# Kernel optimization log

Measured on AMD Instinct MI355X. Metric: run time of the kernel, lower is better.

The kernel has to match this reference:

```python
import jax, jax.numpy as jnp
import numpy as np

KERNEL_SIZE = 7
STRIDE = 1
PADDING = 3
DILATION = 1


def setup_inputs() -> dict:
    key = jax.random.key(0)
    x = jax.random.normal(key, (8, 64, 56, 56), dtype=jnp.float32)
    return {"x": x}


def reference(x):
    """Pairwise subtraction (SAN): center pixel minus each of its k*k
    dilated neighbors, zero-padded borders (pad_mode=0).
    Output: [n, c, k*k, out_h*out_w]."""
    k, s, p, d = KERNEL_SIZE, STRIDE, PADDING, DILATION
    n, c, H, W = x.shape
    out_h = (H + 2 * p - (d * (k - 1) + 1)) // s + 1
    out_w = (W + 2 * p - (d * (k - 1) + 1)) // s + 1
    # centers: unfold with kernel 1, no padding, stride s
    centers = x[:, :, ::s, ::s][:, :, :out_h, :out_w]  # n,c,out_h,out_w
    # neighbors: zero-pad then take k*k strided slices (row-major kernel order
    # to match nn.Unfold)
    xp = jnp.pad(x, ((0, 0), (0, 0), (p, p), (p, p)))
    patches = jnp.stack(
        [
            xp[:, :, i * d : i * d + s * (out_h - 1) + 1 : s,
                     j * d : j * d + s * (out_w - 1) + 1 : s]
            for i in range(k)
            for j in range(k)
        ],
        axis=2,
    )  # n, c, k*k, out_h, out_w
    out = centers.reshape(n, c, 1, out_h * out_w) - patches.reshape(
        n, c, k * k, out_h * out_w
    )
    return out
```

## Files before the change

kernel.cpp:

```cpp
#include <hip/hip_runtime.h>


constexpr int H_ = 56, W_ = 56;
constexpr int KK_  = 49;
constexpr int OHW_ = 3136;
constexpr int PP_  = 63;
constexpr int PR_  = 62;
constexpr int NC_  = 512;
constexpr int LDSN_ = PR_ * PP_;

typedef float f32x4 __attribute__((ext_vector_type(4)));

__global__ __launch_bounds__(256)
void san_kernel(const float* __restrict__ x, float* __restrict__ out) {
    __shared__ float lds[LDSN_];
    const int nc = blockIdx.x;
    const int t  = threadIdx.x;

    #pragma unroll
    for (int i = 0; i < 16; ++i) {
        int j = t + 256 * i;
        if (j < LDSN_) lds[j] = 0.0f;
    }
    __syncthreads();

    const float* plane = x + (size_t)nc * OHW_;

    f32x4 cen0{}, cen1{}, cen2{}, cen3{};
    int ab0 = 0, ab1 = 0, ab2 = 0, ab3 = 0;
    const bool has3 = (t < 16);

#define STAGE(S, CEN, AB)                                           \
    {                                                               \
        int e4 = t + 256 * (S);                                     \
        int oh = e4 / 14, o4 = e4 - oh * 14;                        \
        CEN = *reinterpret_cast<const f32x4*>(plane + e4 * 4);      \
        int lb = (oh + 3) * PP_ + o4 * 4 + 3;                       \
        lds[lb + 0] = CEN[0]; lds[lb + 1] = CEN[1];                 \
        lds[lb + 2] = CEN[2]; lds[lb + 3] = CEN[3];                 \
        AB = oh * PP_ + o4 * 4;                                     \
    }
    STAGE(0, cen0, ab0)
    STAGE(1, cen1, ab1)
    STAGE(2, cen2, ab2)
    if (has3) STAGE(3, cen3, ab3)
#undef STAGE
    __syncthreads();

    float* ob  = out + (size_t)nc * (KK_ * OHW_);
    float* op0 = ob + (size_t)(t      ) * 4;
    float* op1 = ob + (size_t)(t + 256) * 4;
    float* op2 = ob + (size_t)(t + 512) * 4;

    #pragma unroll
    for (int ki = 0; ki < 7; ++ki) {
        #pragma unroll
        for (int kj = 0; kj < 7; ++kj) {
            const int off = ki * PP_ + kj;
            f32x4 r0, r1, r2;
            #pragma unroll
            for (int tt = 0; tt < 4; ++tt) {
                r0[tt] = cen0[tt] - lds[ab0 + off + tt];
                r1[tt] = cen1[tt] - lds[ab1 + off + tt];
                r2[tt] = cen2[tt] - lds[ab2 + off + tt];
            }
            *reinterpret_cast<f32x4*>(op0) = r0;  op0 += OHW_;
            *reinterpret_cast<f32x4*>(op1) = r1;  op1 += OHW_;
            *reinterpret_cast<f32x4*>(op2) = r2;  op2 += OHW_;
        }
    }

    if (has3) {
        float* op3 = ob + (size_t)(t + 768) * 4;
        for (int ki = 0; ki < 7; ++ki) {
            for (int kj = 0; kj < 7; ++kj) {
                int off = ki * PP_ + kj;
                f32x4 r;
                #pragma unroll
                for (int tt = 0; tt < 4; ++tt)
                    r[tt] = cen3[tt] - lds[ab3 + off + tt];
                *reinterpret_cast<f32x4*>(op3) = r;  op3 += OHW_;
            }
        }
    }
}

extern "C" void kernel_launch(void* const* d_in, const int* in_sizes, int n_in,
                              void* d_out, int out_size, void* d_ws, size_t ws_size,
                              hipStream_t stream) {
    const float* x = (const float*)d_in[0];
    float* out = (float*)d_out;
    san_kernel<<<NC_, 256, 0, stream>>>(x, out);
}
```

Measured before the change: 57.44 us.

## Load 12-wide LDS window per row as float4s and reuse across kj

Pads the LDS tile to a 16-byte-aligned pitch with a 4-float halo so staging and neighbor reads become 128-bit LDS accesses. For each kernel row, each thread loads three float4 vectors covering all seven horizontal shifts of its four outputs and reuses them in registers across kj, in place of 196 scalar LDS reads per output group. The separate tail loop for the 16 extra threads is folded into the main unrolled loop with predicated loads and stores. This cuts LDS instruction count, at the cost of more registers and a slightly larger shared buffer.

```diff
diff --git a/kernel.cpp b/kernel.cpp
--- a/kernel.cpp
+++ b/kernel.cpp
@@ -4,46 +4,50 @@
 constexpr int H_ = 56, W_ = 56;
 constexpr int KK_  = 49;
 constexpr int OHW_ = 3136;
-constexpr int PP_  = 63;
-constexpr int PR_  = 62;
 constexpr int NC_  = 512;
-constexpr int LDSN_ = PR_ * PP_;
+constexpr int PITCH = 68;
+constexpr int PROWS = 62;
+constexpr int LHALO = 4;
+constexpr int LDSF  = PROWS * PITCH;
+constexpr int LDS4  = LDSF / 4;
 
 typedef float f32x4 __attribute__((ext_vector_type(4)));
 
+#define WSEL(A, B, C, J) ((J) < 4 ? (A)[(J) & 3] : ((J) < 8 ? (B)[(J) & 3] : (C)[(J) & 3]))
+
 __global__ __launch_bounds__(256)
 void san_kernel(const float* __restrict__ x, float* __restrict__ out) {
-    __shared__ float lds[LDSN_];
+    __shared__ f32x4 lds4[LDS4];
+    float* lds = reinterpret_cast<float*>(lds4);
     const int nc = blockIdx.x;
     const int t  = threadIdx.x;
 
     #pragma unroll
-    for (int i = 0; i < 16; ++i) {
+    for (int i = 0; i < 5; ++i) {
         int j = t + 256 * i;
-        if (j < LDSN_) lds[j] = 0.0f;
+        if (j < LDS4) lds4[j] = f32x4{0.f, 0.f, 0.f, 0.f};
     }
     __syncthreads();
 
     const float* plane = x + (size_t)nc * OHW_;
 
     f32x4 cen0{}, cen1{}, cen2{}, cen3{};
-    int ab0 = 0, ab1 = 0, ab2 = 0, ab3 = 0;
+    int rb0 = 0, rb1 = 0, rb2 = 0, rb3 = 0;
     const bool has3 = (t < 16);
 
-#define STAGE(S, CEN, AB)                                           \
-    {                                                               \
-        int e4 = t + 256 * (S);                                     \
-        int oh = e4 / 14, o4 = e4 - oh * 14;                        \
-        CEN = *reinterpret_cast<const f32x4*>(plane + e4 * 4);      \
-        int lb = (oh + 3) * PP_ + o4 * 4 + 3;                       \
-        lds[lb + 0] = CEN[0]; lds[lb + 1] = CEN[1];                 \
-        lds[lb + 2] = CEN[2]; lds[lb + 3] = CEN[3];                 \
-        AB = oh * PP_ + o4 * 4;                                     \
+#define STAGE(S, CEN, RB)                                            \
+    {                                                                \
+        int e4 = t + 256 * (S);                                      \
+        int oh = e4 / 14, o4 = e4 - oh * 14;                         \
+        CEN = *reinterpret_cast<const f32x4*>(plane + e4 * 4);       \
+        int lb = (oh + 3) * PITCH + LHALO + o4 * 4;                  \
+        *reinterpret_cast<f32x4*>(lds + lb) = CEN;                   \
+        RB = oh * PITCH + (LHALO - 4) + o4 * 4;                      \
     }
-    STAGE(0, cen0, ab0)
-    STAGE(1, cen1, ab1)
-    STAGE(2, cen2, ab2)
-    if (has3) STAGE(3, cen3, ab3)
+    STAGE(0, cen0, rb0)
+    STAGE(1, cen1, rb1)
+    STAGE(2, cen2, rb2)
+    if (has3) STAGE(3, cen3, rb3)
 #undef STAGE
     __syncthreads();
 
@@ -51,36 +55,35 @@
     float* op0 = ob + (size_t)(t      ) * 4;
     float* op1 = ob + (size_t)(t + 256) * 4;
     float* op2 = ob + (size_t)(t + 512) * 4;
+    float* op3 = ob + (size_t)(t + 768) * 4;
 
     #pragma unroll
     for (int ki = 0; ki < 7; ++ki) {
+        const float* w0 = lds + rb0 + ki * PITCH;
+        const float* w1 = lds + rb1 + ki * PITCH;
+        const float* w2 = lds + rb2 + ki * PITCH;
+        const float* w3 = lds + rb3 + ki * PITCH;
+        f32x4 a0 = *(const f32x4*)(w0), b0 = *(const f32x4*)(w0 + 4), c0 = *(const f32x4*)(w0 + 8);
+        f32x4 a1 = *(const f32x4*)(w1), b1 = *(const f32x4*)(w1 + 4), c1 = *(const f32x4*)(w1 + 8);
+        f32x4 a2 = *(const f32x4*)(w2), b2 = *(const f32x4*)(w2 + 4), c2 = *(const f32x4*)(w2 + 8);
+        f32x4 a3{}, b3{}, c3{};
+        if (has3) { a3 = *(const f32x4*)(w3); b3 = *(const f32x4*)(w3 + 4); c3 = *(const f32x4*)(w3 + 8); }
+
         #pragma unroll
         for (int kj = 0; kj < 7; ++kj) {
-            const int off = ki * PP_ + kj;
-            f32x4 r0, r1, r2;
+            f32x4 r0, r1, r2, r3;
             #pragma unroll
             for (int tt = 0; tt < 4; ++tt) {
-                r0[tt] = cen0[tt] - lds[ab0 + off + tt];
-                r1[tt] = cen1[tt] - lds[ab1 + off + tt];
-                r2[tt] = cen2[tt] - lds[ab2 + off + tt];
+                r0[tt] = cen0[tt] - WSEL(a0, b0, c0, kj + 1 + tt);
+                r1[tt] = cen1[tt] - WSEL(a1, b1, c1, kj + 1 + tt);
+                r2[tt] = cen2[tt] - WSEL(a2, b2, c2, kj + 1 + tt);
+                r3[tt] = cen3[tt] - WSEL(a3, b3, c3, kj + 1 + tt);
             }
             *reinterpret_cast<f32x4*>(op0) = r0;  op0 += OHW_;
             *reinterpret_cast<f32x4*>(op1) = r1;  op1 += OHW_;
             *reinterpret_cast<f32x4*>(op2) = r2;  op2 += OHW_;
-        }
-    }
-
-    if (has3) {
-        float* op3 = ob + (size_t)(t + 768) * 4;
-        for (int ki = 0; ki < 7; ++ki) {
-            for (int kj = 0; kj < 7; ++kj) {
-                int off = ki * PP_ + kj;
-                f32x4 r;
-                #pragma unroll
-                for (int tt = 0; tt < 4; ++tt)
-                    r[tt] = cen3[tt] - lds[ab3 + off + tt];
-                *reinterpret_cast<f32x4*>(op3) = r;  op3 += OHW_;
-            }
+            if (has3) *reinterpret_cast<f32x4*>(op3) = r3;
+            op3 += OHW_;
         }
     }
 }
```

Measured after the change: 62.21 us. 1.08x slower.

## Split each plane across seven blocks by kernel row and register-cache window

Applied to the files above, without the earlier changes.

Launches seven blocks per (n,c) plane, one per kernel row ki, so the grid grows from 512 to 3584 blocks and more CUs stay busy on this store-bound kernel. Each thread loads a 10-wide window of the padded plane from LDS into registers once and produces all seven kj outputs from those registers, replacing per-element LDS reads. The cost is that every block re-reads the input plane from global memory and re-zeroes and refills the LDS tile, which multiplies input traffic and setup work by seven.

```diff
diff --git a/kernel.cpp b/kernel.cpp
--- a/kernel.cpp
+++ b/kernel.cpp
@@ -14,8 +14,10 @@
 __global__ __launch_bounds__(256)
 void san_kernel(const float* __restrict__ x, float* __restrict__ out) {
     __shared__ float lds[LDSN_];
-    const int nc = blockIdx.x;
-    const int t  = threadIdx.x;
+    const int bid = blockIdx.x;
+    const int nc  = bid / 7;
+    const int ki  = bid - nc * 7;
+    const int t   = threadIdx.x;
 
     #pragma unroll
     for (int i = 0; i < 16; ++i) {
@@ -27,10 +29,11 @@
     const float* plane = x + (size_t)nc * OHW_;
 
     f32x4 cen0{}, cen1{}, cen2{}, cen3{};
-    int ab0 = 0, ab1 = 0, ab2 = 0, ab3 = 0;
+    int wb0 = 0, wb1 = 0, wb2 = 0, wb3 = 0;
     const bool has3 = (t < 16);
+    const int kio = ki * PP_;
 
-#define STAGE(S, CEN, AB)                                           \
+#define STAGE(S, CEN, WB)                                           \
     {                                                               \
         int e4 = t + 256 * (S);                                     \
         int oh = e4 / 14, o4 = e4 - oh * 14;                        \
@@ -38,50 +41,45 @@
         int lb = (oh + 3) * PP_ + o4 * 4 + 3;                       \
         lds[lb + 0] = CEN[0]; lds[lb + 1] = CEN[1];                 \
         lds[lb + 2] = CEN[2]; lds[lb + 3] = CEN[3];                 \
-        AB = oh * PP_ + o4 * 4;                                     \
+        WB = oh * PP_ + o4 * 4 + kio;                               \
     }
-    STAGE(0, cen0, ab0)
-    STAGE(1, cen1, ab1)
-    STAGE(2, cen2, ab2)
-    if (has3) STAGE(3, cen3, ab3)
+    STAGE(0, cen0, wb0)
+    STAGE(1, cen1, wb1)
+    STAGE(2, cen2, wb2)
+    if (has3) STAGE(3, cen3, wb3)
 #undef STAGE
     __syncthreads();
 
-    float* ob  = out + (size_t)nc * (KK_ * OHW_);
+    float w0[10], w1[10], w2[10], w3[10];
+    #pragma unroll
+    for (int j = 0; j < 10; ++j) {
+        w0[j] = lds[wb0 + j];
+        w1[j] = lds[wb1 + j];
+        w2[j] = lds[wb2 + j];
+        w3[j] = has3 ? lds[wb3 + j] : 0.0f;
+    }
+
+    float* ob  = out + (size_t)nc * (KK_ * OHW_) + (size_t)(ki * 7) * OHW_;
     float* op0 = ob + (size_t)(t      ) * 4;
     float* op1 = ob + (size_t)(t + 256) * 4;
     float* op2 = ob + (size_t)(t + 512) * 4;
+    float* op3 = ob + (size_t)(t + 768) * 4;
 
     #pragma unroll
-    for (int ki = 0; ki < 7; ++ki) {
+    for (int kj = 0; kj < 7; ++kj) {
+        f32x4 r0, r1, r2, r3;
         #pragma unroll
-        for (int kj = 0; kj < 7; ++kj) {
-            const int off = ki * PP_ + kj;
-            f32x4 r0, r1, r2;
-            #pragma unroll
-            for (int tt = 0; tt < 4; ++tt) {
-                r0[tt] = cen0[tt] - lds[ab0 + off + tt];
-                r1[tt] = cen1[tt] - lds[ab1 + off + tt];
-                r2[tt] = cen2[tt] - lds[ab2 + off + tt];
-            }
-            *reinterpret_cast<f32x4*>(op0) = r0;  op0 += OHW_;
-            *reinterpret_cast<f32x4*>(op1) = r1;  op1 += OHW_;
-            *reinterpret_cast<f32x4*>(op2) = r2;  op2 += OHW_;
+        for (int tt = 0; tt < 4; ++tt) {
+            r0[tt] = cen0[tt] - w0[kj + tt];
+            r1[tt] = cen1[tt] - w1[kj + tt];
+            r2[tt] = cen2[tt] - w2[kj + tt];
+            r3[tt] = cen3[tt] - w3[kj + tt];
         }
-    }
-
-    if (has3) {
-        float* op3 = ob + (size_t)(t + 768) * 4;
-        for (int ki = 0; ki < 7; ++ki) {
-            for (int kj = 0; kj < 7; ++kj) {
-                int off = ki * PP_ + kj;
-                f32x4 r;
-                #pragma unroll
-                for (int tt = 0; tt < 4; ++tt)
-                    r[tt] = cen3[tt] - lds[ab3 + off + tt];
-                *reinterpret_cast<f32x4*>(op3) = r;  op3 += OHW_;
-            }
-        }
+        *reinterpret_cast<f32x4*>(op0) = r0;  op0 += OHW_;
+        *reinterpret_cast<f32x4*>(op1) = r1;  op1 += OHW_;
+        *reinterpret_cast<f32x4*>(op2) = r2;  op2 += OHW_;
+        if (has3) *reinterpret_cast<f32x4*>(op3) = r3;
+        op3 += OHW_;
     }
 }
 
@@ -90,5 +88,5 @@
                               hipStream_t stream) {
     const float* x = (const float*)d_in[0];
     float* out = (float*)d_out;
-    san_kernel<<<NC_, 256, 0, stream>>>(x, out);
+    san_kernel<<<NC_ * 7, 256, 0, stream>>>(x, out);
 }
```

Result: no change. 57.63 us (+0.3%).
